# Optimization experiments

Measured on AMD Instinct MI355X. Metric: run time of the kernel, lower is better.

The kernel has to match this reference:

```python
import jax, jax.numpy as jnp
import numpy as np

VOCAB = 512
HID = 1024
BATCH = 64
SEQ = 512


def setup_inputs() -> dict:
    key = jax.random.key(0)
    ks = jax.random.split(key, 9)
    s = 0.01
    return {
        "X": jax.random.normal(ks[0], (BATCH, SEQ, VOCAB), dtype=jnp.float32),
        "state": jnp.zeros((BATCH, HID), dtype=jnp.float32),
        "w_xr": jax.random.normal(ks[1], (VOCAB, HID), dtype=jnp.float32) * s,
        "w_hr": jax.random.normal(ks[2], (HID, HID), dtype=jnp.float32) * s,
        "b_r": jnp.zeros((HID,), dtype=jnp.float32),
        "w_xz": jax.random.normal(ks[3], (VOCAB, HID), dtype=jnp.float32) * s,
        "w_hz": jax.random.normal(ks[4], (HID, HID), dtype=jnp.float32) * s,
        "b_z": jnp.zeros((HID,), dtype=jnp.float32),
        "w_xh": jax.random.normal(ks[5], (VOCAB, HID), dtype=jnp.float32) * s,
        "w_hh": jax.random.normal(ks[6], (HID, HID), dtype=jnp.float32) * s,
        "b_h": jnp.zeros((HID,), dtype=jnp.float32),
        "w_ho": jax.random.normal(ks[7], (HID, VOCAB), dtype=jnp.float32) * s,
        "b_o": jnp.zeros((VOCAB,), dtype=jnp.float32),
    }


def reference(X, state, w_xr, w_hr, b_r, w_xz, w_hz, b_z, w_xh, w_hh, b_h, w_ho, b_o):
    # Precompute all input-to-hidden projections in one big GEMM per gate
    # (mathematically identical to per-step mm, just batched over time).
    xr = jnp.einsum('btv,vh->bth', X, w_xr) + b_r   # [B,T,H]
    xz = jnp.einsum('btv,vh->bth', X, w_xz) + b_z
    xh = jnp.einsum('btv,vh->bth', X, w_xh) + b_h
    # scan over time with hidden-state recurrence
    xs = (jnp.swapaxes(xr, 0, 1), jnp.swapaxes(xz, 0, 1), jnp.swapaxes(xh, 0, 1))  # [T,B,H]

    def step(H, x_t):
        xr_t, xz_t, xh_t = x_t
        r_t = jax.nn.sigmoid(xr_t + H @ w_hr)
        z_t = jax.nn.sigmoid(xz_t + H @ w_hz)
        h_bar = jnp.tanh(xh_t + (r_t * H) @ w_hh)
        H_new = H * z_t + h_bar * (1.0 - z_t)
        o_t = H_new @ w_ho + b_o
        return H_new, o_t

    H_final, outs = jax.lax.scan(step, state, xs)  # outs: [T,B,V]
    T, B, V = outs.shape
    # torch.cat(outputs, dim=0) stacks timesteps along batch dim -> [T*B, V]
    return outs.reshape(T * B, V), H_final
```

## Files before the change

### kernel.cpp

```cpp
#include <hip/hip_runtime.h>
#include <hip/hip_cooperative_groups.h>

namespace cg = cooperative_groups;

#define B_ 64
#define T_ 512
#define V_ 512
#define H_ 1024

typedef short bf16x8 __attribute__((ext_vector_type(8)));
typedef float f32x4 __attribute__((ext_vector_type(4)));

#define EO_PHR 0
#define EO_PHZ (EO_PHR + H_*H_)
#define EO_PHH (EO_PHZ + H_*H_)
#define EO_PXR (EO_PHH + H_*H_)
#define EO_PXZ (EO_PXR + V_*H_)
#define EO_PXH (EO_PXZ + V_*H_)
#define EO_PHO (EO_PXH + V_*H_)
#define EO_HBF (EO_PHO + H_*V_)
#define EO_RHBF (EO_HBF + 2*B_*H_)
#define EO_USEND (EO_RHBF + B_*H_)

__device__ __forceinline__ unsigned short f2bf(float x) {
  unsigned u = __builtin_bit_cast(unsigned, x);
  u = u + 0x7fffu + ((u >> 16) & 1u);
  return (unsigned short)(u >> 16);
}
__device__ __forceinline__ float bf2f(unsigned short b) {
  return __builtin_bit_cast(float, (unsigned)b << 16);
}

__global__ void pack_weights(const float* __restrict__ w_hr, const float* __restrict__ w_hz,
                             const float* __restrict__ w_hh, const float* __restrict__ w_xr,
                             const float* __restrict__ w_xz, const float* __restrict__ w_xh,
                             const float* __restrict__ w_ho, unsigned short* __restrict__ ws) {
  int tid = blockIdx.x * blockDim.x + threadIdx.x;
  const int NH = 64*32*64, NX = 64*16*64, NO = 32*32*64;
  if (tid < 3*NH) {
    int m = tid / NH, idx = tid % NH;
    const float* src = (m==0) ? w_hr : (m==1) ? w_hz : w_hh;
    unsigned short* dst = ws + ((m==0) ? EO_PHR : (m==1) ? EO_PHZ : EO_PHH);
    int l = idx & 63, kt = (idx >> 6) & 31, nt = idx >> 11;
    int n = nt*16 + (l & 15), k0 = kt*32 + (l >> 4)*8;
    #pragma unroll
    for (int j = 0; j < 8; ++j) dst[idx*8 + j] = f2bf(src[(size_t)(k0+j)*H_ + n]);
    return;
  }
  tid -= 3*NH;
  if (tid < 3*NX) {
    int m = tid / NX, idx = tid % NX;
    const float* src = (m==0) ? w_xr : (m==1) ? w_xz : w_xh;
    unsigned short* dst = ws + ((m==0) ? EO_PXR : (m==1) ? EO_PXZ : EO_PXH);
    int l = idx & 63, kt = (idx >> 6) & 15, nt = idx >> 10;
    int n = nt*16 + (l & 15), k0 = kt*32 + (l >> 4)*8;
    #pragma unroll
    for (int j = 0; j < 8; ++j) dst[idx*8 + j] = f2bf(src[(size_t)(k0+j)*H_ + n]);
    return;
  }
  tid -= 3*NX;
  if (tid < NO) {
    int idx = tid;
    unsigned short* dst = ws + EO_PHO;
    int l = idx & 63, kt = (idx >> 6) & 31, nt = idx >> 11;
    int n = nt*16 + (l & 15), k0 = kt*32 + (l >> 4)*8;
    #pragma unroll
    for (int j = 0; j < 8; ++j) dst[idx*8 + j] = f2bf(w_ho[(size_t)(k0+j)*V_ + n]);
  }
}

__device__ __forceinline__ f32x4 hgemm(const unsigned short* __restrict__ A,
                                       const unsigned short* __restrict__ Pk,
                                       int nt, int mt, int lane) {
  f32x4 acc = {0.f, 0.f, 0.f, 0.f};
  const unsigned short* ap = A + (mt*16 + (lane & 15))*H_ + ((lane >> 4)*8);
  const unsigned short* bp = Pk + ((size_t)nt*32*64 + lane)*8;
  #pragma unroll 8
  for (int kt = 0; kt < 32; ++kt) {
    bf16x8 a = *(const bf16x8*)(const void*)(ap + kt*32);
    bf16x8 b = *(const bf16x8*)(const void*)(bp + (size_t)kt*512);
    acc = __builtin_amdgcn_mfma_f32_16x16x32_bf16(a, b, acc, 0, 0, 0);
  }
  return acc;
}

__device__ __forceinline__ f32x4 xgemm(const float* __restrict__ X, int t,
                                       const unsigned short* __restrict__ Pk,
                                       int nt, int mt, int lane) {
  f32x4 acc = {0.f, 0.f, 0.f, 0.f};
  const float* rp = X + (size_t)(mt*16 + (lane & 15))*(T_*V_) + (size_t)t*V_ + ((lane >> 4)*8);
  const unsigned short* bp = Pk + ((size_t)nt*16*64 + lane)*8;
  #pragma unroll 4
  for (int kt = 0; kt < 16; ++kt) {
    float4 x0 = *(const float4*)(rp + kt*32);
    float4 x1 = *(const float4*)(rp + kt*32 + 4);
    bf16x8 a;
    a[0] = (short)f2bf(x0.x); a[1] = (short)f2bf(x0.y);
    a[2] = (short)f2bf(x0.z); a[3] = (short)f2bf(x0.w);
    a[4] = (short)f2bf(x1.x); a[5] = (short)f2bf(x1.y);
    a[6] = (short)f2bf(x1.z); a[7] = (short)f2bf(x1.w);
    bf16x8 b = *(const bf16x8*)(const void*)(bp + (size_t)kt*512);
    acc = __builtin_amdgcn_mfma_f32_16x16x32_bf16(a, b, acc, 0, 0, 0);
  }
  return acc;
}

__global__ void __launch_bounds__(256, 1) gru_main(
    const float* __restrict__ X, const float* __restrict__ state,
    const float* __restrict__ b_r, const float* __restrict__ b_z,
    const float* __restrict__ b_h, const float* __restrict__ b_o,
    float* __restrict__ out, unsigned short* ws) {
  cg::grid_group grid = cg::this_grid();
  const int blk  = blockIdx.x;
  const int wave = threadIdx.x >> 6;
  const int lane = threadIdx.x & 63;
  const int dcol = lane & 15;
  const int drow = (lane >> 4) * 4;

  const unsigned short* Phr = ws + EO_PHR;
  const unsigned short* Phz = ws + EO_PHZ;
  const unsigned short* Phh = ws + EO_PHH;
  const unsigned short* Pxr = ws + EO_PXR;
  const unsigned short* Pxz = ws + EO_PXZ;
  const unsigned short* Pxh = ws + EO_PXH;
  const unsigned short* Pho = ws + EO_PHO;
  unsigned short* HbfBase = ws + EO_HBF;
  unsigned short* RHbf    = ws + EO_RHBF;
  float* fbase = (float*)(ws + EO_USEND);
  float* xrr = fbase;
  float* xzr = fbase + 2*B_*H_;
  float* xhr = fbase + 4*B_*H_;

  f32x4 hreg  = {0.f, 0.f, 0.f, 0.f};
  f32x4 zfrag = {0.f, 0.f, 0.f, 0.f};

  if (blk < 64) {
    int nt = blk, mt = wave;
    #pragma unroll
    for (int q = 0; q < 4; ++q) {
      int b = mt*16 + drow + q, n = nt*16 + dcol;
      float h0 = state[b*H_ + n];
      hreg[q] = h0;
      HbfBase[b*H_ + n] = f2bf(h0);
    }
  } else if (blk < 128) {
    int nt = blk - 64, mt = wave;
    f32x4 acc = xgemm(X, 0, Pxr, nt, mt, lane);
    int n = nt*16 + dcol; float bias = b_r[n];
    #pragma unroll
    for (int q = 0; q < 4; ++q) xrr[(mt*16 + drow + q)*H_ + n] = acc[q] + bias;
  } else if (blk < 192) {
    int nt = blk - 128, mt = wave;
    f32x4 acc = xgemm(X, 0, Pxz, nt, mt, lane);
    int n = nt*16 + dcol; float bias = b_z[n];
    #pragma unroll
    for (int q = 0; q < 4; ++q) xzr[(mt*16 + drow + q)*H_ + n] = acc[q] + bias;
  } else {
    int nt = blk - 192, mt = wave;
    f32x4 acc = xgemm(X, 0, Pxh, nt, mt, lane);
    int n = nt*16 + dcol; float bias = b_h[n];
    #pragma unroll
    for (int q = 0; q < 4; ++q) xhr[(mt*16 + drow + q)*H_ + n] = acc[q] + bias;
  }
  grid.sync();

  for (int i = 0; i < T_; ++i) {
    const unsigned short* Hcur = HbfBase + (i & 1) * (B_*H_);
    unsigned short* Hnxt = HbfBase + ((i + 1) & 1) * (B_*H_);

    if (blk < 64) {
      int nt = blk, mt = wave;
      f32x4 acc = hgemm(Hcur, Phz, nt, mt, lane);
      const float* xz = xzr + (i & 1) * (B_*H_);
      int n = nt*16 + dcol;
      #pragma unroll
      for (int q = 0; q < 4; ++q) {
        int b = mt*16 + drow + q;
        float a = acc[q] + xz[b*H_ + n];
        zfrag[q] = 1.f / (1.f + __expf(-a));
      }
    } else if (blk < 128) {
      int nt = blk - 64, mt = wave;
      f32x4 acc = hgemm(Hcur, Phr, nt, mt, lane);
      const float* xr = xrr + (i & 1) * (B_*H_);
      int n = nt*16 + dcol;
      #pragma unroll
      for (int q = 0; q < 4; ++q) {
        int b = mt*16 + drow + q;
        float r = 1.f / (1.f + __expf(-(acc[q] + xr[b*H_ + n])));
        float hv = bf2f(Hcur[b*H_ + n]);
        RHbf[b*H_ + n] = f2bf(r * hv);
      }
    } else if (blk < 160) {
      if (i > 0) {
        int nt = blk - 128, mt = wave;
        f32x4 acc = hgemm(Hcur, Pho, nt, mt, lane);
        int n = nt*16 + dcol; float bias = b_o[n];
        #pragma unroll
        for (int q = 0; q < 4; ++q) {
          int b = mt*16 + drow + q;
          out[((size_t)(i-1)*B_ + b)*V_ + n] = acc[q] + bias;
        }
      }
    } else if (blk >= 192) {
      if (i + 1 < T_) {
        int nt = blk - 192, mt = wave;
        f32x4 acc = xgemm(X, i + 1, Pxh, nt, mt, lane);
        float* xh = xhr + ((i + 1) & 1) * (B_*H_);
        int n = nt*16 + dcol; float bias = b_h[n];
        #pragma unroll
        for (int q = 0; q < 4; ++q) xh[(mt*16 + drow + q)*H_ + n] = acc[q] + bias;
      }
    }
    grid.sync();

    if (blk < 64) {
      int nt = blk, mt = wave;
      f32x4 acc = hgemm(RHbf, Phh, nt, mt, lane);
      const float* xh = xhr + (i & 1) * (B_*H_);
      int n = nt*16 + dcol;
      #pragma unroll
      for (int q = 0; q < 4; ++q) {
        int b = mt*16 + drow + q;
        float hb = tanhf(acc[q] + xh[b*H_ + n]);
        float z = zfrag[q];
        float hn = hreg[q] * z + hb * (1.f - z);
        hreg[q] = hn;
        Hnxt[b*H_ + n] = f2bf(hn);
      }
    } else if (blk < 128) {
      if (i + 1 < T_) {
        int nt = blk - 64, mt = wave;
        f32x4 acc = xgemm(X, i + 1, Pxr, nt, mt, lane);
        float* xr = xrr + ((i + 1) & 1) * (B_*H_);
        int n = nt*16 + dcol; float bias = b_r[n];
        #pragma unroll
        for (int q = 0; q < 4; ++q) xr[(mt*16 + drow + q)*H_ + n] = acc[q] + bias;
      }
    } else if (blk < 192) {
      if (i + 1 < T_) {
        int nt = blk - 128, mt = wave;
        f32x4 acc = xgemm(X, i + 1, Pxz, nt, mt, lane);
        float* xz = xzr + ((i + 1) & 1) * (B_*H_);
        int n = nt*16 + dcol; float bias = b_z[n];
        #pragma unroll
        for (int q = 0; q < 4; ++q) xz[(mt*16 + drow + q)*H_ + n] = acc[q] + bias;
      }
    }
    grid.sync();
  }

  if (blk < 64) {
    int nt = blk, mt = wave;
    int n = nt*16 + dcol;
    #pragma unroll
    for (int q = 0; q < 4; ++q) {
      int b = mt*16 + drow + q;
      out[(size_t)T_*B_*V_ + b*H_ + n] = hreg[q];
    }
  } else if (blk >= 128 && blk < 160) {
    int nt = blk - 128, mt = wave;
    const unsigned short* Hcur = HbfBase + (T_ & 1) * (B_*H_);
    f32x4 acc = hgemm(Hcur, Pho, nt, mt, lane);
    int n = nt*16 + dcol; float bias = b_o[n];
    #pragma unroll
    for (int q = 0; q < 4; ++q) {
      int b = mt*16 + drow + q;
      out[((size_t)(T_-1)*B_ + b)*V_ + n] = acc[q] + bias;
    }
  }
}

extern "C" void kernel_launch(void* const* d_in, const int* in_sizes, int n_in,
                              void* d_out, int out_size, void* d_ws, size_t ws_size,
                              hipStream_t stream) {
  const float* X     = (const float*)d_in[0];
  const float* state = (const float*)d_in[1];
  const float* w_xr  = (const float*)d_in[2];
  const float* w_hr  = (const float*)d_in[3];
  const float* b_r   = (const float*)d_in[4];
  const float* w_xz  = (const float*)d_in[5];
  const float* w_hz  = (const float*)d_in[6];
  const float* b_z   = (const float*)d_in[7];
  const float* w_xh  = (const float*)d_in[8];
  const float* w_hh  = (const float*)d_in[9];
  const float* b_h   = (const float*)d_in[10];
  const float* w_ho  = (const float*)d_in[11];
  const float* b_o   = (const float*)d_in[12];
  float* outp = (float*)d_out;
  unsigned short* wsp = (unsigned short*)d_ws;

  hipLaunchKernelGGL(pack_weights, dim3(2560), dim3(256), 0, stream,
                     w_hr, w_hz, w_hh, w_xr, w_xz, w_xh, w_ho, wsp);

  void* params[8] = { (void*)&X, (void*)&state, (void*)&b_r, (void*)&b_z,
                      (void*)&b_h, (void*)&b_o, (void*)&outp, (void*)&wsp };
  hipLaunchCooperativeKernel((void*)gru_main, dim3(256), dim3(256), params, 0, stream);
}
```

Measured before the change: 38.92 ms.

## Replace cooperative grid.sync with custom hierarchical atomic grid barrier

Swaps the cooperative-groups grid.sync for a hand-written two-level barrier. Blocks first count into one of 8 group counters, and the last arriver of each group bumps a global counter. The last group then writes release flags that every block spins on with s_sleep. Two alternating barrier sets and monotonic round numbers avoid reset races, and a small kernel zeroes the counters before each launch. The goal is to cut the per-step sync latency of the 1024 barriers in the time loop, at the cost of relying on all 256 blocks being co-resident and on correct memory fencing.

```diff
diff --git a/kernel.cpp b/kernel.cpp
--- a/kernel.cpp
+++ b/kernel.cpp
@@ -1,7 +1,4 @@
 #include <hip/hip_runtime.h>
-#include <hip/hip_cooperative_groups.h>
-
-namespace cg = cooperative_groups;
 
 #define B_ 64
 #define T_ 512
@@ -22,6 +19,15 @@
 #define EO_RHBF (EO_HBF + 2*B_*H_)
 #define EO_USEND (EO_RHBF + B_*H_)
 
+#define B1_GRP 0
+#define B1_GLB 128
+#define B1_REL 144
+#define B2_GRP 272
+#define B2_GLB 400
+#define B2_REL 416
+#define BAR_INTS 544
+__device__ int g_bar[BAR_INTS];
+
 __device__ __forceinline__ unsigned short f2bf(float x) {
   unsigned u = __builtin_bit_cast(unsigned, x);
   u = u + 0x7fffu + ((u >> 16) & 1u);
@@ -29,6 +35,41 @@
 }
 __device__ __forceinline__ float bf2f(unsigned short b) {
   return __builtin_bit_cast(float, (unsigned)b << 16);
+}
+
+__device__ __forceinline__ void gbar(int grpO, int glbO, int relO,
+                                     int g, int round) {
+  __syncthreads();
+  if (threadIdx.x == 0) {
+    __threadfence();
+    int old = __hip_atomic_fetch_add(g_bar + grpO + g * 16, 1,
+                                     __ATOMIC_ACQ_REL, __HIP_MEMORY_SCOPE_AGENT);
+    if ((old & 31) == 31) {
+      int o2 = __hip_atomic_fetch_add(g_bar + glbO, 1,
+                                       __ATOMIC_ACQ_REL, __HIP_MEMORY_SCOPE_AGENT);
+      if ((o2 & 7) == 7) {
+        #pragma unroll
+        for (int k = 0; k < 8; ++k)
+          __hip_atomic_store(g_bar + relO + k * 16, round + 1,
+                             __ATOMIC_RELEASE, __HIP_MEMORY_SCOPE_AGENT);
+      }
+    }
+    while (__hip_atomic_load(g_bar + relO + g * 16,
+                             __ATOMIC_ACQUIRE, __HIP_MEMORY_SCOPE_AGENT) < round + 1)
+      __builtin_amdgcn_s_sleep(2);
+    __threadfence();
+  }
+  __syncthreads();
+}
+__device__ __forceinline__ void bar1(int blk, int round) {
+  gbar(B1_GRP, B1_GLB, B1_REL, blk >> 5, round);
+}
+__device__ __forceinline__ void bar2(int blk, int round) {
+  gbar(B2_GRP, B2_GLB, B2_REL, blk >> 5, round);
+}
+
+__global__ void zero_bar() {
+  if (threadIdx.x < BAR_INTS) g_bar[threadIdx.x] = 0;
 }
 
 __global__ void pack_weights(const float* __restrict__ w_hr, const float* __restrict__ w_hz,
@@ -110,7 +151,6 @@
     const float* __restrict__ b_r, const float* __restrict__ b_z,
     const float* __restrict__ b_h, const float* __restrict__ b_o,
     float* __restrict__ out, unsigned short* ws) {
-  cg::grid_group grid = cg::this_grid();
   const int blk  = blockIdx.x;
   const int wave = threadIdx.x >> 6;
   const int lane = threadIdx.x & 63;
@@ -162,7 +202,7 @@
     #pragma unroll
     for (int q = 0; q < 4; ++q) xhr[(mt*16 + drow + q)*H_ + n] = acc[q] + bias;
   }
-  grid.sync();
+  bar2(blk, 0);
 
   for (int i = 0; i < T_; ++i) {
     const unsigned short* Hcur = HbfBase + (i & 1) * (B_*H_);
@@ -212,7 +252,7 @@
         for (int q = 0; q < 4; ++q) xh[(mt*16 + drow + q)*H_ + n] = acc[q] + bias;
       }
     }
-    grid.sync();
+    bar1(blk, i);
 
     if (blk < 64) {
       int nt = blk, mt = wave;
@@ -247,7 +287,7 @@
         for (int q = 0; q < 4; ++q) xz[(mt*16 + drow + q)*H_ + n] = acc[q] + bias;
       }
     }
-    grid.sync();
+    bar2(blk, i + 1);
   }
 
   if (blk < 64) {
@@ -290,6 +330,7 @@
   float* outp = (float*)d_out;
   unsigned short* wsp = (unsigned short*)d_ws;
 
+  hipLaunchKernelGGL(zero_bar, dim3(1), dim3(576), 0, stream);
   hipLaunchKernelGGL(pack_weights, dim3(2560), dim3(256), 0, stream,
                      w_hr, w_hz, w_hh, w_xr, w_xz, w_xh, w_ho, wsp);
 
```

Result: slower. 59.59 ms (+53.1%).
